# Performance work log

Measured on AMD Instinct MI355X. Metric: run time of the kernel, lower is better.

Reference implementation:

```python
import jax, jax.numpy as jnp
import numpy as np

B, N, FE, FN, MD, HD, KC, P = 16, 64, 1216, 1108, 256, 256, 600, 2

def setup_inputs() -> dict:
    key = jax.random.key(0)
    ks = jax.random.split(key, 20)
    def w(k, shape, fan_in):
        return (jax.random.normal(k, shape, jnp.float32) / np.sqrt(fan_in)).astype(jnp.float32)
    return {
        "edge_features": jax.random.normal(ks[0], (B, N, N, FE), jnp.float32),
        "node_features": jax.random.normal(ks[1], (B, N, FN), jnp.float32),
        "adj_mat": jnp.zeros((B, N, N), jnp.float32),
        "node_labels": jnp.zeros((B, N, KC), jnp.float32),
        "human_nums": jnp.full((B,), 1, jnp.int32),
        "obj_nums": jnp.full((B,), N - 1, jnp.int32),
        "args": 0,
        # feature resize linears
        "W_er": w(ks[2], (MD, FE), FE), "b_er": jnp.zeros((MD,), jnp.float32),
        "W_nr": w(ks[3], (MD, FN), FN), "b_nr": jnp.zeros((MD,), jnp.float32),
        # link fun (GraphConv = stack of 1x1 conv2d): MD -> HD -> 1
        "Wl1": w(ks[4], (HD, MD), MD), "bl1": jnp.zeros((HD,), jnp.float32),
        "Wl2": w(ks[5], (1, HD), HD), "bl2": jnp.zeros((1,), jnp.float32),
        # message fun: Conv1d(2*MD -> MD, k=1) + ReLU, input = cat([h_w, e_vw])
        "Wm": w(ks[6], (MD, 2 * MD), 2 * MD), "bm": jnp.zeros((MD,), jnp.float32),
        # GRU (torch gate order r,z,n); input MD, hidden MD
        "Wi": w(ks[7], (3 * MD, MD), MD), "bi": jnp.zeros((3 * MD,), jnp.float32),
        "Wh": w(ks[8], (3 * MD, MD), MD), "bh": jnp.zeros((3 * MD,), jnp.float32),
        # readout fc
        "Wro": w(ks[9], (KC, MD), MD), "bro": jnp.zeros((KC,), jnp.float32),
    }

def reference(edge_features, node_features, adj_mat, node_labels, human_nums,
              obj_nums, args, W_er, b_er, W_nr, b_nr, Wl1, bl1, Wl2, bl2,
              Wm, bm, Wi, bi, Wh, bh, Wro, bro):
    # resize features to message size, then channel-first like torch permutes
    E0 = jnp.einsum('bvwf,mf->bmvw', edge_features, W_er) + b_er[None, :, None, None]  # [B,MD,N,N]
    Xp = jnp.einsum('bvf,mf->bmv', node_features, W_nr) + b_nr[None, :, None]           # [B,MD,N]

    # pre-mask messages are identical every round: node states are never
    # rewritten in the source and e_vw always reads the original edge_features.
    # M_pre[b,c,i,w] = relu(Wm @ cat(h_w[b,:,w], e_vw[b,:,i,w]) + bm)
    W_hw, W_ev = Wm[:, :MD], Wm[:, MD:]
    Mpre = jax.nn.relu(
        jnp.einsum('cm,bmw->bcw', W_hw, Xp)[:, :, None, :]
        + jnp.einsum('cm,bmiw->bciw', W_ev, E0)
        + bm[None, :, None, None])                                                     # [B,MD,Ni,Nw]

    E = E0  # hidden edge state, round 0
    for _ in range(P):
        h1 = jax.nn.relu(jnp.einsum('hm,bmvw->bhvw', Wl1, E) + bl1[None, :, None, None])
        A = (jnp.einsum('oh,bhvw->bovw', Wl2, h1) + bl2[None, :, None, None])[:, 0]    # [B,N,N]
        S = jax.nn.sigmoid(A)
        Mmask = Mpre * S[:, None, :, :]          # mask message i<-w by sigmoid adj[i,w]
        E = jnp.swapaxes(Mmask, 2, 3)            # E_{r+1}[b,c,w,i] = Mmask[b,c,i,w]
        m_sum = jnp.sum(Mmask, axis=3)           # [B,MD,Ni]

    # GRU update (only last round's output is read out)
    x = jnp.swapaxes(m_sum, 1, 2)                # [B,N,MD]
    h = jnp.swapaxes(Xp, 1, 2)                   # [B,N,MD]
    gi = x @ Wi.T + bi
    gh = h @ Wh.T + bh
    ir, iz, inn = jnp.split(gi, 3, axis=-1)
    hr, hz, hn = jnp.split(gh, 3, axis=-1)
    r = jax.nn.sigmoid(ir + hr)
    z = jax.nn.sigmoid(iz + hz)
    n = jnp.tanh(inn + r * hn)
    h_new = (1.0 - z) * n + z * h
    pred_node_labels = h_new @ Wro.T + bro       # [B,N,KC]
    pred_adj_mat = A                             # last round's link prediction
    return pred_adj_mat, pred_node_labels
```

## Files before the change

### kernel.cpp

```cpp
#include <hip/hip_runtime.h>
#include <cmath>

namespace {

using f16 = _Float16;
typedef f16 f16x8 __attribute__((ext_vector_type(8)));
typedef f16 f16x4 __attribute__((ext_vector_type(4)));
typedef __fp16 h16x2 __attribute__((ext_vector_type(2)));
typedef float f32x4 __attribute__((ext_vector_type(4)));

constexpr int FE = 1216, FN = 1108, MD = 256, KC = 600;
constexpr int PAIRS = 65536, ROWS = 1024;

constexpr size_t OFF_XP    = 0;
constexpr size_t OFF_XPF   = OFF_XP    + 262144;
constexpr size_t OFF_XPH   = OFF_XPF   + 131072;
constexpr size_t OFF_S1    = OFF_XPH   + 262144;
constexpr size_t OFF_S2    = OFF_S1    + 65536;
constexpr size_t OFF_XF    = OFF_S2    + 65536;
constexpr size_t OFF_GI    = OFF_XF    + 131072;
constexpr size_t OFF_GH    = OFF_GI    + 786432;
constexpr size_t OFF_HNF   = OFF_GH    + 786432;
constexpr size_t OFF_WER8  = OFF_HNF   + 131072;
constexpr size_t OFF_WNR8  = OFF_WER8  + 155648;
constexpr size_t OFF_WEV8  = OFF_WNR8  + 147456;
constexpr size_t OFF_WHW8  = OFF_WEV8  + 32768;
constexpr size_t OFF_WL18  = OFF_WHW8  + 32768;
constexpr size_t OFF_WI8   = OFF_WL18  + 32768;
constexpr size_t OFF_WH8   = OFF_WI8   + 98304;
constexpr size_t OFF_WRO8  = OFF_WH8   + 98304;
constexpr size_t OFF_E0H   = OFF_WRO8  + 98304;
constexpr size_t OFF_MPREH = OFF_E0H   + 8388608;

__device__ __forceinline__ float sigmoidf_(float x) { return 1.0f / (1.0f + expf(-x)); }

__device__ __forceinline__ void dma16(const void* g, void* l) {
  __builtin_amdgcn_global_load_lds((const unsigned int*)g, (unsigned int*)l, 16, 0, 0);
}

__device__ __forceinline__ f16x8 cvtp(f32x4 a, f32x4 b) {
  union { h16x2 q[4]; f16x8 h; } u;
  u.q[0] = __builtin_amdgcn_cvt_pkrtz(a[0], a[1]);
  u.q[1] = __builtin_amdgcn_cvt_pkrtz(a[2], a[3]);
  u.q[2] = __builtin_amdgcn_cvt_pkrtz(b[0], b[1]);
  u.q[3] = __builtin_amdgcn_cvt_pkrtz(b[2], b[3]);
  return u.h;
}

__device__ __forceinline__ f16x4 cvtp4(const float4& g) {
  union { h16x2 q[2]; f16x4 h; } u;
  u.q[0] = __builtin_amdgcn_cvt_pkrtz(g.x, g.y);
  u.q[1] = __builtin_amdgcn_cvt_pkrtz(g.z, g.w);
  return u.h;
}

__global__ __launch_bounds__(256) void cast_all(
    const float* __restrict__ W_er, const float* __restrict__ W_nr,
    const float* __restrict__ Wm,   const float* __restrict__ Wl1,
    const float* __restrict__ Wi,   const float* __restrict__ Wh,
    const float* __restrict__ Wro,
    f16* __restrict__ Wer8, f16* __restrict__ Wnr8, f16* __restrict__ Wev8,
    f16* __restrict__ Whw8, f16* __restrict__ Wl18, f16* __restrict__ Wi8,
    f16* __restrict__ Wh8,  f16* __restrict__ Wro8)
{
  int b = blockIdx.x, t = threadIdx.x;
  const float* W; f16* out; int ldw, koff, K, N, Npad, kc, nb;
  if (b < 152)      { W=W_er; out=Wer8; ldw=FE;  koff=0;   K=FE;  N=256; Npad=256; kc=b;     nb=0; }
  else if (b < 296) { b-=152; W=W_nr; out=Wnr8; ldw=FN;  koff=0;   K=FN;  N=256; Npad=256; kc=b; nb=0; }
  else if (b < 328) { b-=296; W=Wm;   out=Wev8; ldw=512; koff=256; K=256; N=256; Npad=256; kc=b; nb=0; }
  else if (b < 360) { b-=328; W=Wm;   out=Whw8; ldw=512; koff=0;   K=256; N=256; Npad=256; kc=b; nb=0; }
  else if (b < 392) { b-=360; W=Wl1;  out=Wl18; ldw=256; koff=0;   K=256; N=256; Npad=256; kc=b; nb=0; }
  else if (b < 488) { b-=392; W=Wi;   out=Wi8;  ldw=256; koff=0;   K=256; N=768; Npad=768; kc=b&31; nb=(b>>5)*256; }
  else if (b < 584) { b-=488; W=Wh;   out=Wh8;  ldw=256; koff=0;   K=256; N=768; Npad=768; kc=b&31; nb=(b>>5)*256; }
  else              { b-=584; W=Wro;  out=Wro8; ldw=256; koff=0;   K=256; N=600; Npad=768; kc=b&31; nb=(b>>5)*256; }
  int n = nb + t;
  if (n >= Npad) return;
  f16x8 h;
#pragma unroll
  for (int j = 0; j < 8; ++j) {
    int k = kc * 8 + j;
    float v = (k < K && n < N) ? W[(size_t)n * ldw + koff + k] : 0.0f;
    h[j] = (f16)v;
  }
  *reinterpret_cast<f16x8*>(out + ((size_t)kc * Npad + n) * 8) = h;
}

__global__ __launch_bounds__(256) void gemm_e0(
    const float* __restrict__ A, const f16* __restrict__ Bp,
    const float* __restrict__ bias, f16* __restrict__ C)
{
  const int tid = threadIdx.x;
  const int wave = tid >> 6, l = tid & 63;
  const int lo = l & 15, hi = l >> 4;
  const int wcol = wave * 64;
  alignas(16) __shared__ char sm[49152];
  f32x4 acc[4][4] = {};
  const size_t arow0 = (size_t)blockIdx.x * 64;

  const char* gsrc0; const char* gsrc1; const char* gsrc2; const char* gsrc3;
  int lo0, lo1, lo2, lo3;
  {
    const int colb = (l & 15) * 16;
#define E0_SRC(J, GP, LO)                                                     \
    { int row = wave*16 + (J)*4 + (l >> 4);                                   \
      int lb  = colb ^ ((row & 7) << 4);                                      \
      GP = (const char*)(A + (arow0 + row) * FE) + lb;                        \
      LO = wave*4096 + (J)*1024; }
    E0_SRC(0, gsrc0, lo0) E0_SRC(1, gsrc1, lo1)
    E0_SRC(2, gsrc2, lo2) E0_SRC(3, gsrc3, lo3)
#undef E0_SRC
  }

#define E0_ISSUE(P)                                                           \
  { char* bb = sm + (P)*16384;                                                \
    dma16(gsrc0, bb + lo0); gsrc0 += 256;                                     \
    dma16(gsrc1, bb + lo1); gsrc1 += 256;                                     \
    dma16(gsrc2, bb + lo2); gsrc2 += 256;                                     \
    dma16(gsrc3, bb + lo3); gsrc3 += 256; }

  E0_ISSUE(0)
  E0_ISSUE(1)

  for (int t = 0; t < 19; ++t) {
    if (t < 18) { asm volatile("s_waitcnt vmcnt(4)" ::: "memory"); }
    else        { asm volatile("s_waitcnt vmcnt(0)" ::: "memory"); }
    __builtin_amdgcn_sched_barrier(0);
    __builtin_amdgcn_s_barrier();
    __builtin_amdgcn_sched_barrier(0);

    f16x8 bf0[4], bf1[4];
#pragma unroll
    for (int n = 0; n < 4; ++n) {
      const int kc0 = t*8 + 0*4 + hi;
      const int kc1 = t*8 + 1*4 + hi;
      bf0[n] = *reinterpret_cast<const f16x8*>(Bp + ((size_t)kc0*256 + (wcol + n*16 + lo)) * 8);
      bf1[n] = *reinterpret_cast<const f16x8*>(Bp + ((size_t)kc1*256 + (wcol + n*16 + lo)) * 8);
    }
    __builtin_amdgcn_sched_barrier(0);
    if (t < 17) { E0_ISSUE((t + 2) % 3) }

    const char* bufp = sm + (t % 3) * 16384;
#pragma unroll
    for (int ks = 0; ks < 2; ++ks) {
      f16x8 af[4];
      const int b0 = ks*128 + hi*32;
#pragma unroll
      for (int m = 0; m < 4; ++m) {
        const int r = m*16 + lo;
        const int x = (r & 7) << 4;
        f32x4 a0 = *reinterpret_cast<const f32x4*>(bufp + r*256 + (b0 ^ x));
        f32x4 a1 = *reinterpret_cast<const f32x4*>(bufp + r*256 + ((b0 + 16) ^ x));
        af[m] = cvtp(a0, a1);
      }
#pragma unroll
      for (int m = 0; m < 4; ++m)
#pragma unroll
        for (int n = 0; n < 4; ++n)
          acc[m][n] = __builtin_amdgcn_mfma_f32_16x16x32_f16(
              af[m], ks == 0 ? bf0[n] : bf1[n], acc[m][n], 0, 0, 0);
    }
  }
#undef E0_ISSUE

  __syncthreads();
#pragma unroll
  for (int m = 0; m < 4; ++m)
#pragma unroll
    for (int n = 0; n < 4; ++n) {
      const int col = wcol + n*16 + lo;
      const float bb = bias[col];
#pragma unroll
      for (int r = 0; r < 4; ++r) {
        const int rl = m*16 + hi*4 + r;
        const int byte = rl*512 + ((col*2) ^ ((rl & 7) << 4));
        *reinterpret_cast<f16*>(sm + byte) = (f16)(acc[m][n][r] + bb);
      }
    }
  __syncthreads();
#pragma unroll
  for (int i = 0; i < 8; ++i) {
    const int lin = i*4096 + tid*16;
    const int row = lin >> 9;
    const int phys = (lin & 511) ^ ((row & 7) << 4);
    f16x8 v = *reinterpret_cast<const f16x8*>(sm + row*512 + phys);
    *reinterpret_cast<f16x8*>((char*)C + arow0*512 + lin) = v;
  }
}

__global__ __launch_bounds__(256) void s1_mpre(
    const f16* __restrict__ E0h, const f16* __restrict__ Bl1,
    const f16* __restrict__ Bev, const float* __restrict__ bl1,
    const float* __restrict__ Wl2, const float* __restrict__ bl2,
    const float* __restrict__ XpH, const float* __restrict__ bm,
    float* __restrict__ S1, f16* __restrict__ Mpreh)
{
  const int blk = blockIdx.x;
  const int tid = threadIdx.x;
  const int wave = tid >> 6, l = tid & 63;
  const int lo = l & 15, hi = l >> 4;
  const int wcol = wave * 64;
  alignas(16) __shared__ char sm[32768];
  __shared__ float red[64][4];
  f32x4 accS[4][4] = {}, accM[4][4] = {};
  const size_t arow0 = (size_t)blk * 64;

  const char* gsrc0; const char* gsrc1;
  int lo0, lo1;
  {
    const int colb = (l & 7) * 16;
#define SM_SRC(J, GP, LO)                                                     \
    { int row = wave*16 + (J)*8 + (l >> 3);                                   \
      int lb  = colb ^ ((row & 7) << 4);                                      \
      GP = (const char*)(E0h + (arow0 + row) * 256) + lb;                     \
      LO = wave*2048 + (J)*1024; }
    SM_SRC(0, gsrc0, lo0) SM_SRC(1, gsrc1, lo1)
#undef SM_SRC
  }
#define SM_ISSUE(P)                                                           \
  { char* bb = sm + (P)*8192;                                                 \
    dma16(gsrc0, bb + lo0); gsrc0 += 128;                                     \
    dma16(gsrc1, bb + lo1); gsrc1 += 128; }

  SM_ISSUE(0)
  __syncthreads();

  for (int t = 0; t < 4; ++t) {
    if (t < 3) { SM_ISSUE((t + 1) & 1) }
    const char* bufp = sm + (t & 1) * 8192;
#pragma unroll
    for (int ks = 0; ks < 2; ++ks) {
      f16x8 af[4], bfS[4], bfM[4];
      const int kc = t*8 + ks*4 + hi;
      const int b0 = ks*64 + hi*16;
#pragma unroll
      for (int m = 0; m < 4; ++m) {
        const int r = m*16 + lo;
        af[m] = *reinterpret_cast<const f16x8*>(bufp + r*128 + (b0 ^ ((r & 7) << 4)));
      }
#pragma unroll
      for (int n = 0; n < 4; ++n) {
        bfS[n] = *reinterpret_cast<const f16x8*>(Bl1 + ((size_t)kc*256 + (wcol + n*16 + lo)) * 8);
        bfM[n] = *reinterpret_cast<const f16x8*>(Bev + ((size_t)kc*256 + (wcol + n*16 + lo)) * 8);
      }
#pragma unroll
      for (int m = 0; m < 4; ++m)
#pragma unroll
        for (int n = 0; n < 4; ++n) {
          accS[m][n] = __builtin_amdgcn_mfma_f32_16x16x32_f16(af[m], bfS[n], accS[m][n], 0, 0, 0);
          accM[m][n] = __builtin_amdgcn_mfma_f32_16x16x32_f16(af[m], bfM[n], accM[m][n], 0, 0, 0);
        }
    }
    __syncthreads();
  }
#undef SM_ISSUE

#pragma unroll
  for (int m = 0; m < 4; ++m) {
#pragma unroll
    for (int r = 0; r < 4; ++r) {
      float p = 0.f;
#pragma unroll
      for (int n = 0; n < 4; ++n) {
        const int col = wcol + n*16 + lo;
        p += Wl2[col] * fmaxf(accS[m][n][r] + bl1[col], 0.0f);
      }
      p += __shfl_xor(p, 1); p += __shfl_xor(p, 2);
      p += __shfl_xor(p, 4); p += __shfl_xor(p, 8);
      if (lo == 0) red[m*16 + hi*4 + r][wave] = p;
    }
  }
  const int rxb = (blk >> 6) * 64;
#pragma unroll
  for (int m = 0; m < 4; ++m)
#pragma unroll
    for (int n = 0; n < 4; ++n) {
      const int col = wcol + n*16 + lo;
      const float bb = bm[col];
#pragma unroll
      for (int r = 0; r < 4; ++r) {
        const int rl = m*16 + hi*4 + r;
        float v = accM[m][n][r] + XpH[(size_t)(rxb + rl)*256 + col] + bb;
        *reinterpret_cast<f16*>(sm + rl*512 + col*2) = (f16)fmaxf(v, 0.0f);
      }
    }
  __syncthreads();
#pragma unroll
  for (int i = 0; i < 8; ++i) {
    const int lin = i*4096 + tid*16;
    f16x8 v = *reinterpret_cast<const f16x8*>(sm + lin);
    *reinterpret_cast<f16x8*>((char*)Mpreh + arow0*512 + lin) = v;
  }
  if (tid < 64)
    S1[arow0 + tid] = sigmoidf_(bl2[0] + red[tid][0] + red[tid][1] + red[tid][2] + red[tid][3]);
}

__global__ __launch_bounds__(256) void attn2_ms(
    const f16* __restrict__ Mpreh, const float* __restrict__ S1,
    const f16* __restrict__ Bl1, const float* __restrict__ bl1,
    const float* __restrict__ Wl2, const float* __restrict__ bl2,
    float* __restrict__ adj, f16* __restrict__ xf)
{
  const int blk = blockIdx.x;
  const int b = blk >> 6, v = blk & 63;
  const int tid = threadIdx.x;
  const int wave = tid >> 6, l = tid & 63;
  const int lo = l & 15, hi = l >> 4;
  const int wcol = wave * 64;
  __shared__ f16 As[2][64][72];
  __shared__ float red[64][4];
  __shared__ float s1s[64];
  __shared__ float s2s[64];
  f32x4 acc[4][4] = {};
  const int rr0 = tid >> 3, part = tid & 7;
  const size_t pbase = (size_t)b * 4096 + v;
  f16x8 ga, gb;

  if (tid < 64) s1s[tid] = S1[pbase + (size_t)tid * 64];
  __syncthreads();

#define A2_LOAD(T)                                                              \
  { ga = *reinterpret_cast<const f16x8*>(Mpreh + (pbase + (size_t)rr0*64)*256 + (T)*64 + part*8);     \
    gb = *reinterpret_cast<const f16x8*>(Mpreh + (pbase + (size_t)(rr0+32)*64)*256 + (T)*64 + part*8); }
#define A2_WRITE(BUF)                                                           \
  { f16 sa = (f16)s1s[rr0], sb = (f16)s1s[rr0 + 32];                            \
    f16x8 ha = ga, hb = gb;                                                     \
    _Pragma("unroll") for (int j = 0; j < 8; ++j) { ha[j] *= sa; hb[j] *= sb; } \
    *reinterpret_cast<f16x8*>(&As[BUF][rr0][part*8]) = ha;                      \
    *reinterpret_cast<f16x8*>(&As[BUF][rr0 + 32][part*8]) = hb; }

  A2_LOAD(0); A2_WRITE(0);
  for (int t = 0; t < 4; ++t) {
    __syncthreads();
    if (t < 3) A2_LOAD(t + 1);
    const int cur = t & 1;
#pragma unroll
    for (int ks = 0; ks < 2; ++ks) {
      f16x8 af[4], bf[4];
      const int kc = t*8 + ks*4 + hi;
#pragma unroll
      for (int m = 0; m < 4; ++m)
        af[m] = *reinterpret_cast<const f16x8*>(&As[cur][m*16 + lo][ks*32 + hi*8]);
#pragma unroll
      for (int n = 0; n < 4; ++n)
        bf[n] = *reinterpret_cast<const f16x8*>(Bl1 + ((size_t)kc*256 + (wcol + n*16 + lo)) * 8);
#pragma unroll
      for (int m = 0; m < 4; ++m)
#pragma unroll
        for (int n = 0; n < 4; ++n)
          acc[m][n] = __builtin_amdgcn_mfma_f32_16x16x32_f16(af[m], bf[n], acc[m][n], 0, 0, 0);
    }
    if (t < 3) A2_WRITE(cur ^ 1);
  }
#undef A2_LOAD
#undef A2_WRITE
#pragma unroll
  for (int m = 0; m < 4; ++m) {
#pragma unroll
    for (int r = 0; r < 4; ++r) {
      float p = 0.f;
#pragma unroll
      for (int n = 0; n < 4; ++n) {
        const int col = wcol + n*16 + lo;
        p += Wl2[col] * fmaxf(acc[m][n][r] + bl1[col], 0.0f);
      }
      p += __shfl_xor(p, 1); p += __shfl_xor(p, 2);
      p += __shfl_xor(p, 4); p += __shfl_xor(p, 8);
      if (lo == 0) red[m*16 + hi*4 + r][wave] = p;
    }
  }
  __syncthreads();
  if (tid < 64) {
    float s = bl2[0] + red[tid][0] + red[tid][1] + red[tid][2] + red[tid][3];
    adj[(size_t)b*4096 + (size_t)v*64 + tid] = s;
    s2s[tid] = sigmoidf_(s);
  }
  __syncthreads();
  const int c = tid;
  const f16* mp = Mpreh + (size_t)blk * 64 * 256 + c;
  float accx = 0.f;
#pragma unroll 8
  for (int w = 0; w < 64; ++w)
    accx += (float)mp[(size_t)w * 256] * s2s[w];
  xf[(size_t)blk * 256 + c] = (f16)accx;
}

__global__ __launch_bounds__(256) void xp_xph16(
    const float* __restrict__ A, const f16* __restrict__ Bnr,
    const float* __restrict__ b_nr, const f16* __restrict__ Bhw,
    float* __restrict__ Xp, f16* __restrict__ Xpf, float* __restrict__ XpH)
{
  const int tid = threadIdx.x;
  const int wave = tid >> 6, l = tid & 63;
  const int lo = l & 15, hi = l >> 4;
  const int wcol = wave * 64;
  __shared__ f16 As[2][16][72];
  __shared__ f16 XpS[16][264];
  f32x4 acc[4] = {};
  const size_t arow0 = (size_t)blockIdx.x * 16;
  const int srow = tid >> 4, spart = tid & 15;
  const float* abase = A + (arow0 + srow) * FN;
  float4 g;
  const float4 z4 = make_float4(0.f, 0.f, 0.f, 0.f);

#define XQ_LOAD(T)                                                          \
  { int kb = (T)*64 + spart*4;                                              \
    g = (kb + 4 <= FN) ? *(const float4*)(abase + kb) : z4; }
#define XQ_WRITE(BUF)                                                       \
  { *reinterpret_cast<f16x4*>(&As[BUF][srow][spart*4]) = cvtp4(g); }

  XQ_LOAD(0); XQ_WRITE(0);
  for (int t = 0; t < 18; ++t) {
    __syncthreads();
    if (t < 17) XQ_LOAD(t + 1);
    const int cur = t & 1;
#pragma unroll
    for (int ks = 0; ks < 2; ++ks) {
      const int kc = t*8 + ks*4 + hi;
      f16x8 af = *reinterpret_cast<const f16x8*>(&As[cur][lo][ks*32 + hi*8]);
      f16x8 bf[4];
#pragma unroll
      for (int n = 0; n < 4; ++n)
        bf[n] = *reinterpret_cast<const f16x8*>(Bnr + ((size_t)kc*256 + (wcol + n*16 + lo)) * 8);
#pragma unroll
      for (int n = 0; n < 4; ++n)
        acc[n] = __builtin_amdgcn_mfma_f32_16x16x32_f16(af, bf[n], acc[n], 0, 0, 0);
    }
    if (t < 17) XQ_WRITE(cur ^ 1);
  }
#undef XQ_LOAD
#undef XQ_WRITE
#pragma unroll
  for (int n = 0; n < 4; ++n) {
    const int col = wcol + n*16 + lo;
    const float bb = b_nr[col];
#pragma unroll
    for (int r = 0; r < 4; ++r) {
      const size_t row = arow0 + hi*4 + r;
      float v = acc[n][r] + bb;
      Xp[row * 256 + col] = v;
      f16 hv = (f16)v;
      Xpf[row * 256 + col] = hv;
      XpS[hi*4 + r][col] = hv;
    }
  }
  __syncthreads();
  f32x4 acch[4] = {};
  for (int t = 0; t < 4; ++t) {
#pragma unroll
    for (int ks = 0; ks < 2; ++ks) {
      const int kc = t*8 + ks*4 + hi;
      f16x8 af = *reinterpret_cast<const f16x8*>(&XpS[lo][t*64 + ks*32 + hi*8]);
      f16x8 bf[4];
#pragma unroll
      for (int n = 0; n < 4; ++n)
        bf[n] = *reinterpret_cast<const f16x8*>(Bhw + ((size_t)kc*256 + (wcol + n*16 + lo)) * 8);
#pragma unroll
      for (int n = 0; n < 4; ++n)
        acch[n] = __builtin_amdgcn_mfma_f32_16x16x32_f16(af, bf[n], acch[n], 0, 0, 0);
    }
  }
#pragma unroll
  for (int n = 0; n < 4; ++n) {
    const int col = wcol + n*16 + lo;
#pragma unroll
    for (int r = 0; r < 4; ++r)
      XpH[(arow0 + hi*4 + r) * 256 + col] = acch[n][r];
  }
}

__global__ __launch_bounds__(256) void gigh16(
    const f16* __restrict__ xf, const f16* __restrict__ Xpf,
    const f16* __restrict__ Wi8, const f16* __restrict__ Wh8,
    const float* __restrict__ bi, const float* __restrict__ bh,
    float* __restrict__ gi, float* __restrict__ gh)
{
  const int rb = blockIdx.x;
  int cb = blockIdx.y;
  const f16* A; const f16* Bp; const float* bias; float* C;
  if (cb < 3) { A = xf;  Bp = Wi8; bias = bi; C = gi; }
  else        { A = Xpf; Bp = Wh8; bias = bh; C = gh; cb -= 3; }
  const int tid = threadIdx.x;
  const int wave = tid >> 6, l = tid & 63;
  const int lo = l & 15, hi = l >> 4;
  const int wcol = cb * 256 + wave * 64;
  __shared__ f16 As[16][264];
  f32x4 acc[4] = {};
  const size_t arow0 = (size_t)rb * 16;

#pragma unroll
  for (int i = 0; i < 2; ++i) {
    int idx = i * 256 + tid;
    int rr = idx >> 5, part = idx & 31;
    *reinterpret_cast<f16x8*>(&As[rr][part*8]) =
        *reinterpret_cast<const f16x8*>(A + (arow0 + rr)*256 + part*8);
  }
  __syncthreads();

  for (int t = 0; t < 4; ++t) {
#pragma unroll
    for (int ks = 0; ks < 2; ++ks) {
      const int kc = t*8 + ks*4 + hi;
      f16x8 af = *reinterpret_cast<const f16x8*>(&As[lo][t*64 + ks*32 + hi*8]);
      f16x8 bf[4];
#pragma unroll
      for (int n = 0; n < 4; ++n)
        bf[n] = *reinterpret_cast<const f16x8*>(Bp + ((size_t)kc*768 + (wcol + n*16 + lo)) * 8);
#pragma unroll
      for (int n = 0; n < 4; ++n)
        acc[n] = __builtin_amdgcn_mfma_f32_16x16x32_f16(af, bf[n], acc[n], 0, 0, 0);
    }
  }
#pragma unroll
  for (int n = 0; n < 4; ++n) {
    const int col = wcol + n*16 + lo;
    const float bb = bias[col];
#pragma unroll
    for (int r = 0; r < 4; ++r)
      C[(arow0 + hi*4 + r) * 768 + col] = acc[n][r] + bb;
  }
}

__global__ __launch_bounds__(256) void labels_gru16(
    const float* __restrict__ gi, const float* __restrict__ gh,
    const float* __restrict__ Xp, const f16* __restrict__ Wro8,
    const float* __restrict__ bro, float* __restrict__ labels)
{
  const int rb = blockIdx.x, cb = blockIdx.y;
  const int tid = threadIdx.x;
  const int wave = tid >> 6, l = tid & 63;
  const int lo = l & 15, hi = l >> 4;
  const int wcol = cb * 256 + wave * 64;
  __shared__ f16 As[16][264];
  f32x4 acc[4] = {};
  const size_t arow0 = (size_t)rb * 16;

  {
    const int rr = tid >> 4, c0 = (tid & 15) * 16;
    const float* gir = gi + (arow0 + rr) * 768;
    const float* ghr = gh + (arow0 + rr) * 768;
    const float* xpr = Xp + (arow0 + rr) * 256;
#pragma unroll
    for (int j = 0; j < 16; ++j) {
      const int c = c0 + j;
      float r = sigmoidf_(gir[c] + ghr[c]);
      float z = sigmoidf_(gir[256 + c] + ghr[256 + c]);
      float n = tanhf(gir[512 + c] + r * ghr[512 + c]);
      float h = xpr[c];
      As[rr][c] = (f16)((1.0f - z) * n + z * h);
    }
  }
  __syncthreads();

  for (int t = 0; t < 4; ++t) {
#pragma unroll
    for (int ks = 0; ks < 2; ++ks) {
      const int kc = t*8 + ks*4 + hi;
      f16x8 af = *reinterpret_cast<const f16x8*>(&As[lo][t*64 + ks*32 + hi*8]);
      f16x8 bf[4];
#pragma unroll
      for (int n = 0; n < 4; ++n)
        bf[n] = *reinterpret_cast<const f16x8*>(Wro8 + ((size_t)kc*768 + (wcol + n*16 + lo)) * 8);
#pragma unroll
      for (int n = 0; n < 4; ++n)
        acc[n] = __builtin_amdgcn_mfma_f32_16x16x32_f16(af, bf[n], acc[n], 0, 0, 0);
    }
  }
#pragma unroll
  for (int n = 0; n < 4; ++n) {
    const int col = wcol + n*16 + lo;
    if (col < KC) {
      const float bb = bro[col];
#pragma unroll
      for (int r = 0; r < 4; ++r)
        labels[(arow0 + hi*4 + r) * (size_t)KC + col] = acc[n][r] + bb;
    }
  }
}

}

extern "C" void kernel_launch(void* const* d_in, const int* in_sizes, int n_in,
                              void* d_out, int out_size, void* d_ws, size_t ws_size,
                              hipStream_t stream)
{
  const float* ef   = (const float*)d_in[0];
  const float* nf   = (const float*)d_in[1];
  const float* W_er = (const float*)d_in[7];
  const float* b_er = (const float*)d_in[8];
  const float* W_nr = (const float*)d_in[9];
  const float* b_nr = (const float*)d_in[10];
  const float* Wl1  = (const float*)d_in[11];
  const float* bl1  = (const float*)d_in[12];
  const float* Wl2  = (const float*)d_in[13];
  const float* bl2  = (const float*)d_in[14];
  const float* Wm   = (const float*)d_in[15];
  const float* bm   = (const float*)d_in[16];
  const float* Wi   = (const float*)d_in[17];
  const float* bi   = (const float*)d_in[18];
  const float* Wh   = (const float*)d_in[19];
  const float* bh   = (const float*)d_in[20];
  const float* Wro  = (const float*)d_in[21];
  const float* bro  = (const float*)d_in[22];

  float* ws = (float*)d_ws;
  float* Xp    = ws + OFF_XP;
  f16*   Xpf   = (f16*)(ws + OFF_XPF);
  float* XpH   = ws + OFF_XPH;
  float* S1    = ws + OFF_S1;
  f16*   xf    = (f16*)(ws + OFF_XF);
  float* gi    = ws + OFF_GI;
  float* gh    = ws + OFF_GH;
  f16*   Wer8  = (f16*)(ws + OFF_WER8);
  f16*   Wnr8  = (f16*)(ws + OFF_WNR8);
  f16*   Wev8  = (f16*)(ws + OFF_WEV8);
  f16*   Whw8  = (f16*)(ws + OFF_WHW8);
  f16*   Wl18  = (f16*)(ws + OFF_WL18);
  f16*   Wi8   = (f16*)(ws + OFF_WI8);
  f16*   Wh8   = (f16*)(ws + OFF_WH8);
  f16*   Wro8  = (f16*)(ws + OFF_WRO8);
  f16*   E0h   = (f16*)(ws + OFF_E0H);
  f16*   Mpreh = (f16*)(ws + OFF_MPREH);
  float* adj    = (float*)d_out;
  float* labels = (float*)d_out + PAIRS;

  dim3 blk(256);

  cast_all<<<dim3(680), blk, 0, stream>>>(W_er, W_nr, Wm, Wl1, Wi, Wh, Wro,
                                          Wer8, Wnr8, Wev8, Whw8, Wl18, Wi8, Wh8, Wro8);
  xp_xph16<<<dim3(64), blk, 0, stream>>>(nf, Wnr8, b_nr, Whw8, Xp, Xpf, XpH);
  gemm_e0<<<dim3(PAIRS / 64), blk, 0, stream>>>(ef, Wer8, b_er, E0h);
  s1_mpre<<<dim3(PAIRS / 64), blk, 0, stream>>>(E0h, Wl18, Wev8, bl1, Wl2, bl2,
                                                XpH, bm, S1, Mpreh);
  attn2_ms<<<dim3(PAIRS / 64), blk, 0, stream>>>(Mpreh, S1, Wl18, bl1, Wl2, bl2,
                                                 adj, xf);
  gigh16<<<dim3(64, 6), blk, 0, stream>>>(xf, Xpf, Wi8, Wh8, bi, bh, gi, gh);
  labels_gru16<<<dim3(64, 3), blk, 0, stream>>>(gi, gh, Xp, Wro8, bro, labels);
}
```

Baseline: 219.5 us.

## Fuse E0 resize GEMM with link and message GEMMs in one kernel

Merges gemm_e0 and s1_mpre into a single kernel. The E0 tile stays in shared memory as f16 and feeds the Wl1 and Wm(edge) GEMMs directly, so it is no longer written to and re-read from global memory. The two follow-on GEMMs now run one after the other to limit register pressure. This removes one launch and 32 MB of global traffic, at the cost of a longer per-block critical path and possibly lower occupancy.

New measurement: 203.3 us. 7.4% less time.

```diff
diff --git a/kernel.cpp b/kernel.cpp
--- a/kernel.cpp
+++ b/kernel.cpp
@@ -85,204 +85,185 @@
   *reinterpret_cast<f16x8*>(out + ((size_t)kc * Npad + n) * 8) = h;
 }
 
-__global__ __launch_bounds__(256) void gemm_e0(
-    const float* __restrict__ A, const f16* __restrict__ Bp,
-    const float* __restrict__ bias, f16* __restrict__ C)
+__global__ __launch_bounds__(256) void e0_sm(
+    const float* __restrict__ A, const f16* __restrict__ Ber,
+    const float* __restrict__ b_er,
+    const f16* __restrict__ Bl1, const f16* __restrict__ Bev,
+    const float* __restrict__ bl1, const float* __restrict__ Wl2,
+    const float* __restrict__ bl2,
+    const float* __restrict__ XpH, const float* __restrict__ bm,
+    float* __restrict__ S1, f16* __restrict__ Mpreh)
 {
   const int tid = threadIdx.x;
   const int wave = tid >> 6, l = tid & 63;
   const int lo = l & 15, hi = l >> 4;
   const int wcol = wave * 64;
   alignas(16) __shared__ char sm[49152];
-  f32x4 acc[4][4] = {};
+  __shared__ float red[64][4];
   const size_t arow0 = (size_t)blockIdx.x * 64;
 
-  const char* gsrc0; const char* gsrc1; const char* gsrc2; const char* gsrc3;
-  int lo0, lo1, lo2, lo3;
   {
-    const int colb = (l & 15) * 16;
+    f32x4 acc[4][4] = {};
+    const char* gsrc0; const char* gsrc1; const char* gsrc2; const char* gsrc3;
+    int lo0, lo1, lo2, lo3;
+    {
+      const int colb = (l & 15) * 16;
 #define E0_SRC(J, GP, LO)                                                     \
-    { int row = wave*16 + (J)*4 + (l >> 4);                                   \
-      int lb  = colb ^ ((row & 7) << 4);                                      \
-      GP = (const char*)(A + (arow0 + row) * FE) + lb;                        \
-      LO = wave*4096 + (J)*1024; }
-    E0_SRC(0, gsrc0, lo0) E0_SRC(1, gsrc1, lo1)
-    E0_SRC(2, gsrc2, lo2) E0_SRC(3, gsrc3, lo3)
+      { int row = wave*16 + (J)*4 + (l >> 4);                                 \
+        int lb  = colb ^ ((row & 7) << 4);                                    \
+        GP = (const char*)(A + (arow0 + row) * FE) + lb;                      \
+        LO = wave*4096 + (J)*1024; }
+      E0_SRC(0, gsrc0, lo0) E0_SRC(1, gsrc1, lo1)
+      E0_SRC(2, gsrc2, lo2) E0_SRC(3, gsrc3, lo3)
 #undef E0_SRC
-  }
-
+    }
 #define E0_ISSUE(P)                                                           \
-  { char* bb = sm + (P)*16384;                                                \
-    dma16(gsrc0, bb + lo0); gsrc0 += 256;                                     \
-    dma16(gsrc1, bb + lo1); gsrc1 += 256;                                     \
-    dma16(gsrc2, bb + lo2); gsrc2 += 256;                                     \
-    dma16(gsrc3, bb + lo3); gsrc3 += 256; }
-
-  E0_ISSUE(0)
-  E0_ISSUE(1)
-
-  for (int t = 0; t < 19; ++t) {
-    if (t < 18) { asm volatile("s_waitcnt vmcnt(4)" ::: "memory"); }
-    else        { asm volatile("s_waitcnt vmcnt(0)" ::: "memory"); }
-    __builtin_amdgcn_sched_barrier(0);
-    __builtin_amdgcn_s_barrier();
-    __builtin_amdgcn_sched_barrier(0);
-
-    f16x8 bf0[4], bf1[4];
-#pragma unroll
-    for (int n = 0; n < 4; ++n) {
-      const int kc0 = t*8 + 0*4 + hi;
-      const int kc1 = t*8 + 1*4 + hi;
-      bf0[n] = *reinterpret_cast<const f16x8*>(Bp + ((size_t)kc0*256 + (wcol + n*16 + lo)) * 8);
-      bf1[n] = *reinterpret_cast<const f16x8*>(Bp + ((size_t)kc1*256 + (wcol + n*16 + lo)) * 8);
-    }
-    __builtin_amdgcn_sched_barrier(0);
-    if (t < 17) { E0_ISSUE((t + 2) % 3) }
-
-    const char* bufp = sm + (t % 3) * 16384;
-#pragma unroll
-    for (int ks = 0; ks < 2; ++ks) {
-      f16x8 af[4];
-      const int b0 = ks*128 + hi*32;
-#pragma unroll
-      for (int m = 0; m < 4; ++m) {
-        const int r = m*16 + lo;
-        const int x = (r & 7) << 4;
-        f32x4 a0 = *reinterpret_cast<const f32x4*>(bufp + r*256 + (b0 ^ x));
-        f32x4 a1 = *reinterpret_cast<const f32x4*>(bufp + r*256 + ((b0 + 16) ^ x));
-        af[m] = cvtp(a0, a1);
-      }
-#pragma unroll
-      for (int m = 0; m < 4; ++m)
-#pragma unroll
-        for (int n = 0; n < 4; ++n)
-          acc[m][n] = __builtin_amdgcn_mfma_f32_16x16x32_f16(
-              af[m], ks == 0 ? bf0[n] : bf1[n], acc[m][n], 0, 0, 0);
-    }
-  }
+    { char* bb = sm + (P)*16384;                                              \
+      dma16(gsrc0, bb + lo0); gsrc0 += 256;                                   \
+      dma16(gsrc1, bb + lo1); gsrc1 += 256;                                   \
+      dma16(gsrc2, bb + lo2); gsrc2 += 256;                                   \
+      dma16(gsrc3, bb + lo3); gsrc3 += 256; }
+
+    E0_ISSUE(0)
+    E0_ISSUE(1)
+
+    for (int t = 0; t < 19; ++t) {
+      if (t < 18) { asm volatile("s_waitcnt vmcnt(4)" ::: "memory"); }
+      else        { asm volatile("s_waitcnt vmcnt(0)" ::: "memory"); }
+      __builtin_amdgcn_sched_barrier(0);
+      __builtin_amdgcn_s_barrier();
+      __builtin_amdgcn_sched_barrier(0);
+
+      f16x8 bf0[4], bf1[4];
+#pragma unroll
+      for (int n = 0; n < 4; ++n) {
+        const int kc0 = t*8 + 0*4 + hi;
+        const int kc1 = t*8 + 1*4 + hi;
+        bf0[n] = *reinterpret_cast<const f16x8*>(Ber + ((size_t)kc0*256 + (wcol + n*16 + lo)) * 8);
+        bf1[n] = *reinterpret_cast<const f16x8*>(Ber + ((size_t)kc1*256 + (wcol + n*16 + lo)) * 8);
+      }
+      __builtin_amdgcn_sched_barrier(0);
+      if (t < 17) { E0_ISSUE((t + 2) % 3) }
+
+      const char* bufp = sm + (t % 3) * 16384;
+#pragma unroll
+      for (int ks = 0; ks < 2; ++ks) {
+        f16x8 af[4];
+        const int b0 = ks*128 + hi*32;
+#pragma unroll
+        for (int m = 0; m < 4; ++m) {
+          const int r = m*16 + lo;
+          const int x = (r & 7) << 4;
+          f32x4 a0 = *reinterpret_cast<const f32x4*>(bufp + r*256 + (b0 ^ x));
+          f32x4 a1 = *reinterpret_cast<const f32x4*>(bufp + r*256 + ((b0 + 16) ^ x));
+          af[m] = cvtp(a0, a1);
+        }
+#pragma unroll
+        for (int m = 0; m < 4; ++m)
+#pragma unroll
+          for (int n = 0; n < 4; ++n)
+            acc[m][n] = __builtin_amdgcn_mfma_f32_16x16x32_f16(
+                af[m], ks == 0 ? bf0[n] : bf1[n], acc[m][n], 0, 0, 0);
+      }
+    }
 #undef E0_ISSUE
 
-  __syncthreads();
-#pragma unroll
-  for (int m = 0; m < 4; ++m)
-#pragma unroll
-    for (int n = 0; n < 4; ++n) {
-      const int col = wcol + n*16 + lo;
-      const float bb = bias[col];
-#pragma unroll
-      for (int r = 0; r < 4; ++r) {
-        const int rl = m*16 + hi*4 + r;
-        const int byte = rl*512 + ((col*2) ^ ((rl & 7) << 4));
-        *reinterpret_cast<f16*>(sm + byte) = (f16)(acc[m][n][r] + bb);
-      }
-    }
-  __syncthreads();
-#pragma unroll
-  for (int i = 0; i < 8; ++i) {
-    const int lin = i*4096 + tid*16;
-    const int row = lin >> 9;
-    const int phys = (lin & 511) ^ ((row & 7) << 4);
-    f16x8 v = *reinterpret_cast<const f16x8*>(sm + row*512 + phys);
-    *reinterpret_cast<f16x8*>((char*)C + arow0*512 + lin) = v;
-  }
-}
-
-__global__ __launch_bounds__(256) void s1_mpre(
-    const f16* __restrict__ E0h, const f16* __restrict__ Bl1,
-    const f16* __restrict__ Bev, const float* __restrict__ bl1,
-    const float* __restrict__ Wl2, const float* __restrict__ bl2,
-    const float* __restrict__ XpH, const float* __restrict__ bm,
-    float* __restrict__ S1, f16* __restrict__ Mpreh)
-{
-  const int blk = blockIdx.x;
-  const int tid = threadIdx.x;
-  const int wave = tid >> 6, l = tid & 63;
-  const int lo = l & 15, hi = l >> 4;
-  const int wcol = wave * 64;
-  alignas(16) __shared__ char sm[32768];
-  __shared__ float red[64][4];
-  f32x4 accS[4][4] = {}, accM[4][4] = {};
-  const size_t arow0 = (size_t)blk * 64;
-
-  const char* gsrc0; const char* gsrc1;
-  int lo0, lo1;
-  {
-    const int colb = (l & 7) * 16;
-#define SM_SRC(J, GP, LO)                                                     \
-    { int row = wave*16 + (J)*8 + (l >> 3);                                   \
-      int lb  = colb ^ ((row & 7) << 4);                                      \
-      GP = (const char*)(E0h + (arow0 + row) * 256) + lb;                     \
-      LO = wave*2048 + (J)*1024; }
-    SM_SRC(0, gsrc0, lo0) SM_SRC(1, gsrc1, lo1)
-#undef SM_SRC
-  }
-#define SM_ISSUE(P)                                                           \
-  { char* bb = sm + (P)*8192;                                                 \
-    dma16(gsrc0, bb + lo0); gsrc0 += 128;                                     \
-    dma16(gsrc1, bb + lo1); gsrc1 += 128; }
-
-  SM_ISSUE(0)
-  __syncthreads();
-
-  for (int t = 0; t < 4; ++t) {
-    if (t < 3) { SM_ISSUE((t + 1) & 1) }
-    const char* bufp = sm + (t & 1) * 8192;
-#pragma unroll
-    for (int ks = 0; ks < 2; ++ks) {
-      f16x8 af[4], bfS[4], bfM[4];
-      const int kc = t*8 + ks*4 + hi;
-      const int b0 = ks*64 + hi*16;
-#pragma unroll
-      for (int m = 0; m < 4; ++m) {
-        const int r = m*16 + lo;
-        af[m] = *reinterpret_cast<const f16x8*>(bufp + r*128 + (b0 ^ ((r & 7) << 4)));
-      }
-#pragma unroll
-      for (int n = 0; n < 4; ++n) {
-        bfS[n] = *reinterpret_cast<const f16x8*>(Bl1 + ((size_t)kc*256 + (wcol + n*16 + lo)) * 8);
-        bfM[n] = *reinterpret_cast<const f16x8*>(Bev + ((size_t)kc*256 + (wcol + n*16 + lo)) * 8);
-      }
-#pragma unroll
-      for (int m = 0; m < 4; ++m)
-#pragma unroll
-        for (int n = 0; n < 4; ++n) {
-          accS[m][n] = __builtin_amdgcn_mfma_f32_16x16x32_f16(af[m], bfS[n], accS[m][n], 0, 0, 0);
-          accM[m][n] = __builtin_amdgcn_mfma_f32_16x16x32_f16(af[m], bfM[n], accM[m][n], 0, 0, 0);
-        }
-    }
     __syncthreads();
-  }
-#undef SM_ISSUE
-
-#pragma unroll
-  for (int m = 0; m < 4; ++m) {
-#pragma unroll
-    for (int r = 0; r < 4; ++r) {
-      float p = 0.f;
+#pragma unroll
+    for (int m = 0; m < 4; ++m)
 #pragma unroll
       for (int n = 0; n < 4; ++n) {
         const int col = wcol + n*16 + lo;
-        p += Wl2[col] * fmaxf(accS[m][n][r] + bl1[col], 0.0f);
-      }
-      p += __shfl_xor(p, 1); p += __shfl_xor(p, 2);
-      p += __shfl_xor(p, 4); p += __shfl_xor(p, 8);
-      if (lo == 0) red[m*16 + hi*4 + r][wave] = p;
-    }
-  }
-  const int rxb = (blk >> 6) * 64;
-#pragma unroll
-  for (int m = 0; m < 4; ++m)
-#pragma unroll
-    for (int n = 0; n < 4; ++n) {
-      const int col = wcol + n*16 + lo;
-      const float bb = bm[col];
+        const float bb = b_er[col];
+#pragma unroll
+        for (int r = 0; r < 4; ++r) {
+          const int rl = m*16 + hi*4 + r;
+          const int byte = rl*512 + ((col*2) ^ ((rl & 7) << 4));
+          *reinterpret_cast<f16*>(sm + byte) = (f16)(acc[m][n][r] + bb);
+        }
+      }
+  }
+  __syncthreads();
+
+  {
+    f32x4 accS[4][4] = {};
+    for (int t = 0; t < 4; ++t) {
+#pragma unroll
+      for (int ks = 0; ks < 2; ++ks) {
+        const int kc = t*8 + ks*4 + hi;
+        const int b0 = t*128 + ks*64 + hi*16;
+        f16x8 af[4], bf[4];
+#pragma unroll
+        for (int m = 0; m < 4; ++m) {
+          const int r = m*16 + lo;
+          af[m] = *reinterpret_cast<const f16x8*>(sm + r*512 + (b0 ^ ((r & 7) << 4)));
+        }
+#pragma unroll
+        for (int n = 0; n < 4; ++n)
+          bf[n] = *reinterpret_cast<const f16x8*>(Bl1 + ((size_t)kc*256 + (wcol + n*16 + lo)) * 8);
+#pragma unroll
+        for (int m = 0; m < 4; ++m)
+#pragma unroll
+          for (int n = 0; n < 4; ++n)
+            accS[m][n] = __builtin_amdgcn_mfma_f32_16x16x32_f16(af[m], bf[n], accS[m][n], 0, 0, 0);
+      }
+    }
+#pragma unroll
+    for (int m = 0; m < 4; ++m) {
 #pragma unroll
       for (int r = 0; r < 4; ++r) {
-        const int rl = m*16 + hi*4 + r;
-        float v = accM[m][n][r] + XpH[(size_t)(rxb + rl)*256 + col] + bb;
-        *reinterpret_cast<f16*>(sm + rl*512 + col*2) = (f16)fmaxf(v, 0.0f);
-      }
-    }
+        float p = 0.f;
+#pragma unroll
+        for (int n = 0; n < 4; ++n) {
+          const int col = wcol + n*16 + lo;
+          p += Wl2[col] * fmaxf(accS[m][n][r] + bl1[col], 0.0f);
+        }
+        p += __shfl_xor(p, 1); p += __shfl_xor(p, 2);
+        p += __shfl_xor(p, 4); p += __shfl_xor(p, 8);
+        if (lo == 0) red[m*16 + hi*4 + r][wave] = p;
+      }
+    }
+  }
+
+  {
+    f32x4 accM[4][4] = {};
+    for (int t = 0; t < 4; ++t) {
+#pragma unroll
+      for (int ks = 0; ks < 2; ++ks) {
+        const int kc = t*8 + ks*4 + hi;
+        const int b0 = t*128 + ks*64 + hi*16;
+        f16x8 af[4], bf[4];
+#pragma unroll
+        for (int m = 0; m < 4; ++m) {
+          const int r = m*16 + lo;
+          af[m] = *reinterpret_cast<const f16x8*>(sm + r*512 + (b0 ^ ((r & 7) << 4)));
+        }
+#pragma unroll
+        for (int n = 0; n < 4; ++n)
+          bf[n] = *reinterpret_cast<const f16x8*>(Bev + ((size_t)kc*256 + (wcol + n*16 + lo)) * 8);
+#pragma unroll
+        for (int m = 0; m < 4; ++m)
+#pragma unroll
+          for (int n = 0; n < 4; ++n)
+            accM[m][n] = __builtin_amdgcn_mfma_f32_16x16x32_f16(af[m], bf[n], accM[m][n], 0, 0, 0);
+      }
+    }
+    __syncthreads();
+    const int rxb = (blockIdx.x >> 6) * 64;
+#pragma unroll
+    for (int m = 0; m < 4; ++m)
+#pragma unroll
+      for (int n = 0; n < 4; ++n) {
+        const int col = wcol + n*16 + lo;
+        const float bb = bm[col];
+#pragma unroll
+        for (int r = 0; r < 4; ++r) {
+          const int rl = m*16 + hi*4 + r;
+          float v = accM[m][n][r] + XpH[(size_t)(rxb + rl)*256 + col] + bb;
+          *reinterpret_cast<f16*>(sm + rl*512 + col*2) = (f16)fmaxf(v, 0.0f);
+        }
+      }
+  }
   __syncthreads();
 #pragma unroll
   for (int i = 0; i < 8; ++i) {
@@ -618,7 +599,6 @@
   f16*   Wi8   = (f16*)(ws + OFF_WI8);
   f16*   Wh8   = (f16*)(ws + OFF_WH8);
   f16*   Wro8  = (f16*)(ws + OFF_WRO8);
-  f16*   E0h   = (f16*)(ws + OFF_E0H);
   f16*   Mpreh = (f16*)(ws + OFF_MPREH);
   float* adj    = (float*)d_out;
   float* labels = (float*)d_out + PAIRS;
@@ -628,9 +608,9 @@
   cast_all<<<dim3(680), blk, 0, stream>>>(W_er, W_nr, Wm, Wl1, Wi, Wh, Wro,
                                           Wer8, Wnr8, Wev8, Whw8, Wl18, Wi8, Wh8, Wro8);
   xp_xph16<<<dim3(64), blk, 0, stream>>>(nf, Wnr8, b_nr, Whw8, Xp, Xpf, XpH);
-  gemm_e0<<<dim3(PAIRS / 64), blk, 0, stream>>>(ef, Wer8, b_er, E0h);
-  s1_mpre<<<dim3(PAIRS / 64), blk, 0, stream>>>(E0h, Wl18, Wev8, bl1, Wl2, bl2,
-                                                XpH, bm, S1, Mpreh);
+  e0_sm<<<dim3(PAIRS / 64), blk, 0, stream>>>(ef, Wer8, b_er, Wl18, Wev8,
+                                              bl1, Wl2, bl2, XpH, bm,
+                                              S1, Mpreh);
   attn2_ms<<<dim3(PAIRS / 64), blk, 0, stream>>>(Mpreh, S1, Wl18, bl1, Wl2, bl2,
                                                  adj, xf);
   gigh16<<<dim3(64, 6), blk, 0, stream>>>(xf, Xpf, Wi8, Wh8, bi, bh, gi, gh);
```
